# Performance work log

Hardware: AMD Instinct MI355X
Metric: run time of the kernel (lower is better)

Reference implementation:

```python
import jax, jax.numpy as jnp
import numpy as np

D_MODEL = 768
NUM_HEADS = 48
HEAD_CH = D_MODEL // NUM_HEADS  # 16
INNER = 3 * D_MODEL
BATCH = 2
SEQLEN = 2048
SKIP = 1.0
EPS = 1e-6


def setup_inputs() -> dict:
    key = jax.random.key(0)
    ks = jax.random.split(key, 9)
    s_in = 1.0 / np.sqrt(D_MODEL)
    s_out = 1.0 / np.sqrt(D_MODEL)
    return {
        "inputs": jax.random.normal(ks[0], (BATCH, SEQLEN, D_MODEL), jnp.float32),
        "w_in": jax.random.normal(ks[1], (INNER, D_MODEL), jnp.float32) * s_in,
        "b_in": jax.random.normal(ks[2], (INNER,), jnp.float32) * 0.01,
        "w_sf": jax.random.normal(ks[3], (INNER, 3), jnp.float32) * 0.3,  # depthwise conv kernel
        "b_sf": jax.random.normal(ks[4], (INNER,), jnp.float32) * 0.01,
        "h": jax.random.normal(ks[5], (NUM_HEADS, SEQLEN), jnp.float32) * 0.02,  # long filter
        "norm_w": jnp.ones((D_MODEL,), jnp.float32),
        "w_out": jax.random.normal(ks[6], (D_MODEL, D_MODEL), jnp.float32) * s_out,
        "b_out": jax.random.normal(ks[7], (D_MODEL,), jnp.float32) * 0.01,
    }


def reference(inputs, w_in, b_in, w_sf, b_sf, h, norm_w, w_out, b_out):
    B, L, D = inputs.shape
    N, HC = NUM_HEADS, HEAD_CH
    # in_proj: [B, L, 3D]
    u = jnp.einsum('bld,ed->ble', inputs, w_in) + b_in
    u = jnp.transpose(u, (0, 2, 1))  # [B, 3D, L]
    # causal depthwise conv1d, kernel 3, left pad 2
    up = jnp.pad(u, ((0, 0), (0, 0), (2, 0)))
    uc = (w_sf[:, 0:1] * up[:, :, 0:L]
          + w_sf[:, 1:2] * up[:, :, 1:L + 1]
          + w_sf[:, 2:3] * up[:, :, 2:L + 2]
          + b_sf[:, None])  # [B, 3D, L]
    uc = uc.reshape(B, N, 3 * HC, L)
    x0 = uc[:, :, 0:HC, :]            # q  [B, N, HC, L]
    x1 = uc[:, :, HC:2 * HC, :]       # k  [B, N, HC, L]
    v = uc[:, :, 2 * HC:3 * HC, :]    # v  [B, N, HC, L]
    # outer product: [B, HC_i, HC_j, N, L]
    kv = jnp.einsum('bnil,bnjl->bijnl', x1, v)
    # FFT long convolution with h [N, L], broadcast over b,i,j
    fft_size = 2 * L
    k_f = jnp.fft.rfft(h, n=fft_size) / fft_size        # [N, L+1]
    u_f = jnp.fft.rfft(kv, n=fft_size, axis=-1)         # [B, HC, HC, N, L+1]
    hkv = jnp.fft.irfft(u_f * k_f, n=fft_size, axis=-1, norm='forward')[..., :L]
    # contract with q: [B, L, N, HC_j]
    qhkv = jnp.einsum('bijnl,bnil->blnj', hkv, x0)
    y = qhkv.reshape(B, L, D)
    # RMSNorm
    ms = jnp.mean(jnp.square(y), axis=-1, keepdims=True)
    y = y * jax.lax.rsqrt(ms + EPS) * norm_w
    # out_proj + skip
    y = jnp.einsum('bld,ed->ble', y, w_out) + b_out
    return y + inputs * SKIP
```

## Files before the change

kernel.cpp:

```cpp
#include <hip/hip_runtime.h>
#include <hip/hip_bf16.h>
#include <stdint.h>

typedef __bf16 bf16;
typedef __bf16 bf16x4 __attribute__((ext_vector_type(4)));
typedef __bf16 bf16x8 __attribute__((ext_vector_type(8)));
typedef float f32x4 __attribute__((ext_vector_type(4)));
typedef float f32x16 __attribute__((ext_vector_type(16)));

#define D_MODEL 768
#define NUM_HEADS 48
#define HEAD_CH 16
#define INNER 2304
#define BATCH 2
#define SEQLEN 2048
#define M_ROWS (BATCH * SEQLEN)
#define EPSF 1e-6f

__device__ inline void gload_lds16(const void* g, void* l) {
  __builtin_amdgcn_global_load_lds((__attribute__((address_space(1))) void*)(g),
                                   (__attribute__((address_space(3))) void*)(l),
                                   16, 0, 0);
}

__global__ __launch_bounds__(256) void cvt2_f32_bf16(
    const float* __restrict__ a, bf16* __restrict__ da, int na4,
    const float* __restrict__ b, bf16* __restrict__ db, int nb4) {
  int j = blockIdx.x * 256 + threadIdx.x;
  const float* s;
  bf16* d;
  if (j < na4) {
    s = a; d = da;
  } else {
    j -= na4;
    if (j >= nb4) return;
    s = b; d = db;
  }
  const float4 v = ((const float4*)s)[j];
  bf16x4 o;
  o[0] = (bf16)v.x; o[1] = (bf16)v.y; o[2] = (bf16)v.z; o[3] = (bf16)v.w;
  ((bf16x4*)d)[j] = o;
}

__global__ __launch_bounds__(256) void cvt_f32_bf16(
    const float* __restrict__ src, bf16* __restrict__ dst, int n4) {
  const int i = blockIdx.x * 256 + threadIdx.x;
  if (i < n4) {
    const float4 v = ((const float4*)src)[i];
    bf16x4 o;
    o[0] = (bf16)v.x; o[1] = (bf16)v.y; o[2] = (bf16)v.z; o[3] = (bf16)v.w;
    ((bf16x4*)dst)[i] = o;
  }
}

template <int TM, int TN, int NCOLS, bool ADD_SKIP, typename CT>
__global__ __launch_bounds__(256) void gemm_bt(
    const bf16* __restrict__ A, const bf16* __restrict__ W,
    const float* __restrict__ bias, const float* __restrict__ skip,
    CT* __restrict__ C, int K) {
  constexpr int MI = TM / 32;
  constexpr int NI = TN / 32;
  __shared__ __align__(16) bf16 As[TM * 32];
  __shared__ __align__(16) bf16 Bs[TN * 32];
  const int t = threadIdx.x;
  const int lane = t & 63, w = t >> 6;
  const int wm = (w >> 1) * (TM / 2), wn = (w & 1) * (TN / 2);
  const int row16 = lane & 15, quad = lane >> 4;
  const int m0 = blockIdx.x * TM, n0 = blockIdx.y * TN;

  f32x4 zero4 = {0.f, 0.f, 0.f, 0.f};
  f32x4 acc[MI][NI];
#pragma unroll
  for (int mi = 0; mi < MI; ++mi)
#pragma unroll
    for (int ni = 0; ni < NI; ++ni) acc[mi][ni] = zero4;

  const int arow = t >> 2;
  const int acol = (t & 3) * 8;
  const bf16* Ab = A + (size_t)m0 * K;
  const bf16* Wb = W + (size_t)n0 * K;

  for (int kt = 0; kt < K; kt += 32) {
    gload_lds16(Ab + (size_t)arow * K + kt + acol, As + t * 8);
    if (TM == 128)
      gload_lds16(Ab + (size_t)(64 + arow) * K + kt + acol, As + 2048 + t * 8);
    gload_lds16(Wb + (size_t)arow * K + kt + acol, Bs + t * 8);
    if (TN == 128)
      gload_lds16(Wb + (size_t)(64 + arow) * K + kt + acol, Bs + 2048 + t * 8);
    __syncthreads();

    bf16x8 af[MI], wf[NI];
#pragma unroll
    for (int mi = 0; mi < MI; ++mi)
      af[mi] = *(const bf16x8*)&As[(wm + mi * 16 + row16) * 32 + quad * 8];
#pragma unroll
    for (int ni = 0; ni < NI; ++ni)
      wf[ni] = *(const bf16x8*)&Bs[(wn + ni * 16 + row16) * 32 + quad * 8];
#pragma unroll
    for (int mi = 0; mi < MI; ++mi)
#pragma unroll
      for (int ni = 0; ni < NI; ++ni)
        acc[mi][ni] = __builtin_amdgcn_mfma_f32_16x16x32_bf16(
            af[mi], wf[ni], acc[mi][ni], 0, 0, 0);
    __syncthreads();
  }

#pragma unroll
  for (int mi = 0; mi < MI; ++mi) {
#pragma unroll
    for (int ni = 0; ni < NI; ++ni) {
      const int col = n0 + wn + ni * 16 + row16;
      const float bv = bias[col];
#pragma unroll
      for (int r = 0; r < 4; ++r) {
        const int row = m0 + wm + mi * 16 + quad * 4 + r;
        float v = acc[mi][ni][r] + bv;
        if (ADD_SKIP) v += skip[(size_t)row * NCOLS + col];
        C[(size_t)row * NCOLS + col] = (CT)v;
      }
    }
  }
}

__global__ __launch_bounds__(256) void conv_qkv(
    const bf16* __restrict__ u, const float* __restrict__ w_sf,
    const float* __restrict__ b_sf, bf16* __restrict__ qq,
    bf16* __restrict__ kk, bf16* __restrict__ vv) {
  const int nh = blockIdx.x, b = blockIdx.y, lc = blockIdx.z;
  const int l0 = lc * 128;
  __shared__ __align__(8) bf16 ut[130 * 48];
  const int t = threadIdx.x;
  for (int i = t; i < 130 * 12; i += 256) {
    const int lr = i / 12, qd = i % 12;
    const int l = l0 - 2 + lr;
    uint2 val;
    val.x = 0u; val.y = 0u;
    if (l >= 0)
      val = *(const uint2*)&u[(size_t)(b * SEQLEN + l) * INNER + nh * 48 + qd * 4];
    *(uint2*)&ut[lr * 48 + qd * 4] = val;
  }
  __syncthreads();
  const size_t bn = (size_t)(b * NUM_HEADS + nh);
#pragma unroll
  for (int s = 0; s < 2; ++s) {
    bf16* dst = (s == 0) ? qq : kk;
    const int cb = s * 16;
    for (int i = t; i < 128 * 16; i += 256) {
      const int c = i & 15, lr = i >> 4;
      const int e = nh * 48 + cb + c;
      const float val = w_sf[e * 3 + 0] * (float)ut[lr * 48 + cb + c] +
                        w_sf[e * 3 + 1] * (float)ut[(lr + 1) * 48 + cb + c] +
                        w_sf[e * 3 + 2] * (float)ut[(lr + 2) * 48 + cb + c] +
                        b_sf[e];
      dst[(bn * SEQLEN + l0 + lr) * 16 + c] = (bf16)val;
    }
  }
  for (int i = t; i < 128 * 16; i += 256) {
    const int lr = i & 127, c = i >> 7;
    const int e = nh * 48 + 32 + c;
    const float val = w_sf[e * 3 + 0] * (float)ut[lr * 48 + 32 + c] +
                      w_sf[e * 3 + 1] * (float)ut[(lr + 1) * 48 + 32 + c] +
                      w_sf[e * 3 + 2] * (float)ut[(lr + 2) * 48 + 32 + c] +
                      b_sf[e];
    vv[(bn * 16 + c) * SEQLEN + l0 + lr] = (bf16)val;
  }
}

__global__ __launch_bounds__(256) void attn_kernel(
    const bf16* __restrict__ qq, const bf16* __restrict__ kk,
    const bf16* __restrict__ vv, const float* __restrict__ hg,
    float* __restrict__ y) {
  const int nh = blockIdx.x, b = blockIdx.y;
  const int q32 = (int)gridDim.z - 1 - (int)blockIdx.z;
  const int l0 = q32 * 32;
  __shared__ __align__(16) float hs[32 + SEQLEN];
  __shared__ __align__(16) bf16 st[4 * 32 * 40];
  const int t = threadIdx.x;
  const int n4 = (l0 + 64) >> 2;
  for (int i = t; i < n4; i += 256) {
    float4 val = {0.f, 0.f, 0.f, 0.f};
    if (i >= 8) val = ((const float4*)(hg + nh * SEQLEN))[i - 8];
    ((float4*)hs)[i] = val;
  }
  __syncthreads();

  const int w = t >> 6, lane = t & 63;
  const int l31 = lane & 31, hi = lane >> 5;
  const int row16 = lane & 15, quad = lane >> 4;
  const size_t bn = (size_t)(b * NUM_HEADS + nh);
  const bf16* qb = qq + bn * SEQLEN * 16;
  const bf16* kb = kk + bn * SEQLEN * 16;
  const bf16* vb = vv + bn * 16 * SEQLEN;

  bf16x8 zf;
#pragma unroll
  for (int j = 0; j < 8; ++j) zf[j] = (bf16)0.f;
  const f32x4 zacc4 = {0.f, 0.f, 0.f, 0.f};
  f32x16 zacc16;
#pragma unroll
  for (int j = 0; j < 16; ++j) zacc16[j] = 0.f;

  const bf16x8 qf = *(const bf16x8*)&qb[(l0 + l31) * 16 + hi * 8];

  f32x4 o0 = zacc4, o1 = zacc4;
  bf16* sw = &st[w * 32 * 40];

  int mc = w * 32;
  bf16x8 kf = zf, vf = zf;
  if (mc <= l0) {
    kf = *(const bf16x8*)&kb[(mc + l31) * 16 + hi * 8];
    vf = *(const bf16x8*)&vb[row16 * SEQLEN + mc + quad * 8];
  }
  for (; mc <= l0; mc += 128) {
    const int mn = mc + 128;
    bf16x8 kf2 = zf, vf2 = zf;
    if (mn <= l0) {
      kf2 = *(const bf16x8*)&kb[(mn + l31) * 16 + hi * 8];
      vf2 = *(const bf16x8*)&vb[row16 * SEQLEN + mn + quad * 8];
    }
    f32x16 s = __builtin_amdgcn_mfma_f32_32x32x16_bf16(kf, qf, zacc16, 0, 0, 0);

    const int d0 = 32 + (l0 - mc) + l31 - 4 * hi;
#pragma unroll
    for (int g = 0; g < 4; ++g) {
      const float* hp = &hs[d0 - 8 * g - 3];
      bf16x4 pk;
      pk[0] = (bf16)(s[4 * g + 0] * hp[3]);
      pk[1] = (bf16)(s[4 * g + 1] * hp[2]);
      pk[2] = (bf16)(s[4 * g + 2] * hp[1]);
      pk[3] = (bf16)(s[4 * g + 3] * hp[0]);
      *(bf16x4*)&sw[l31 * 40 + 8 * g + 4 * hi] = pk;
    }
    asm volatile("s_waitcnt lgkmcnt(0)" ::: "memory");
    const bf16x8 sf0 = *(const bf16x8*)&sw[row16 * 40 + quad * 8];
    const bf16x8 sf1 = *(const bf16x8*)&sw[(row16 + 16) * 40 + quad * 8];
    o0 = __builtin_amdgcn_mfma_f32_16x16x32_bf16(sf0, vf, o0, 0, 0, 0);
    o1 = __builtin_amdgcn_mfma_f32_16x16x32_bf16(sf1, vf, o1, 0, 0, 0);
    asm volatile("" ::: "memory");
    kf = kf2; vf = vf2;
  }

  float* ob = (float*)&st[w * 32 * 40];
#pragma unroll
  for (int r = 0; r < 4; ++r) {
    ob[(quad * 4 + r) * 16 + row16] = o0[r];
    ob[(quad * 4 + r + 16) * 16 + row16] = o1[r];
  }
  __syncthreads();
  for (int i = t; i < 32 * 16; i += 256) {
    const int l = i >> 4, j = i & 15;
    float sum = 0.f;
#pragma unroll
    for (int ww = 0; ww < 4; ++ww)
      sum += ((const float*)&st[ww * 32 * 40])[l * 16 + j];
    y[((size_t)(b * SEQLEN + l0 + l) * NUM_HEADS + nh) * 16 + j] = sum;
  }
}

__global__ __launch_bounds__(256) void rmsnorm_k(
    const float* __restrict__ y, const float* __restrict__ nw,
    bf16* __restrict__ yn) {
  const int row = blockIdx.x;
  const int t = threadIdx.x;
  const float* yr = y + (size_t)row * D_MODEL;
  const float v0 = yr[t];
  const float v1 = yr[t + 256];
  const float v2 = yr[t + 512];
  float ss = v0 * v0 + v1 * v1 + v2 * v2;
#pragma unroll
  for (int off = 32; off >= 1; off >>= 1) ss += __shfl_down(ss, off, 64);
  __shared__ float red[4];
  if ((t & 63) == 0) red[t >> 6] = ss;
  __syncthreads();
  const float tot = red[0] + red[1] + red[2] + red[3];
  const float r = rsqrtf(tot * (1.f / 768.f) + EPSF);
  bf16* yo = yn + (size_t)row * D_MODEL;
  yo[t] = (bf16)(v0 * r * nw[t]);
  yo[t + 256] = (bf16)(v1 * r * nw[t + 256]);
  yo[t + 512] = (bf16)(v2 * r * nw[t + 512]);
}

extern "C" void kernel_launch(void* const* d_in, const int* in_sizes, int n_in,
                              void* d_out, int out_size, void* d_ws,
                              size_t ws_size, hipStream_t stream) {
  const float* inputs = (const float*)d_in[0];
  const float* w_in = (const float*)d_in[1];
  const float* b_in = (const float*)d_in[2];
  const float* w_sf = (const float*)d_in[3];
  const float* b_sf = (const float*)d_in[4];
  const float* hb = (const float*)d_in[5];
  const float* norm_w = (const float*)d_in[6];
  const float* w_out = (const float*)d_in[7];
  const float* b_out = (const float*)d_in[8];

  char* ws = (char*)d_ws;
  const size_t U_B = (size_t)M_ROWS * INNER * 2;
  const size_t V_B = (size_t)BATCH * NUM_HEADS * HEAD_CH * SEQLEN * 2;
  const size_t SLOT_B = (size_t)M_ROWS * D_MODEL * 2;
  bf16* u = (bf16*)(ws);
  bf16* wout16 = (bf16*)(ws);
  bf16* yn = (bf16*)(ws + (2 << 20));
  bf16* v = (bf16*)(ws + U_B);
  bf16* in16 = (bf16*)(ws + U_B + V_B);
  bf16* k16 = in16;
  bf16* win16 = (bf16*)(ws + U_B + V_B + SLOT_B);
  bf16* q16 = win16;
  float* y = (float*)d_out;
  float* out = (float*)d_out;

  const int n4_in = M_ROWS * D_MODEL / 4;
  const int n4_win = INNER * D_MODEL / 4;
  const int n4_wout = D_MODEL * D_MODEL / 4;
  hipLaunchKernelGGL(cvt2_f32_bf16, dim3((n4_in + n4_win + 255) / 256),
                     dim3(256), 0, stream, inputs, in16, n4_in, w_in, win16,
                     n4_win);

  hipLaunchKernelGGL((gemm_bt<128, 128, INNER, false, bf16>), dim3(32, 18),
                     dim3(256), 0, stream, in16, win16, b_in,
                     (const float*)nullptr, u, 768);
  hipLaunchKernelGGL(conv_qkv, dim3(48, 2, 16), dim3(256), 0, stream, u, w_sf,
                     b_sf, q16, k16, v);
  hipLaunchKernelGGL(cvt_f32_bf16, dim3((n4_wout + 255) / 256), dim3(256), 0,
                     stream, w_out, wout16, n4_wout);
  hipLaunchKernelGGL(attn_kernel, dim3(48, 2, 64), dim3(256), 0, stream, q16,
                     k16, v, hb, y);
  hipLaunchKernelGGL(rmsnorm_k, dim3(M_ROWS), dim3(256), 0, stream, y, norm_w,
                     yn);
  hipLaunchKernelGGL((gemm_bt<64, 64, D_MODEL, true, float>), dim3(64, 12),
                     dim3(256), 0, stream, yn, wout16, b_out, inputs, out,
                     768);
}
```

Before: 190.4 us.

## Pair causal query tiles per block and store attention output in bf16

Each attention block now handles two query tiles, z and 63-z, with two waves per tile. This balances the causal workload across blocks and halves the grid. The intermediate y buffer is written as bf16 to a workspace slot instead of fp32, which cuts the write and read traffic between the attention and RMSNorm kernels. The cost is some reduced precision before normalization, plus a workspace offset that must not overlap live buffers.

```diff
diff --git a/kernel.cpp b/kernel.cpp
--- a/kernel.cpp
+++ b/kernel.cpp
@@ -169,14 +169,14 @@
 __global__ __launch_bounds__(256) void attn_kernel(
     const bf16* __restrict__ qq, const bf16* __restrict__ kk,
     const bf16* __restrict__ vv, const float* __restrict__ hg,
-    float* __restrict__ y) {
+    bf16* __restrict__ y) {
   const int nh = blockIdx.x, b = blockIdx.y;
-  const int q32 = (int)gridDim.z - 1 - (int)blockIdx.z;
-  const int l0 = q32 * 32;
+  const int z = blockIdx.z;
+  const int qa = z, qb = 63 - z;
   __shared__ __align__(16) float hs[32 + SEQLEN];
   __shared__ __align__(16) bf16 st[4 * 32 * 40];
   const int t = threadIdx.x;
-  const int n4 = (l0 + 64) >> 2;
+  const int n4 = (qb * 32 + 64) >> 2;
   for (int i = t; i < n4; i += 256) {
     float4 val = {0.f, 0.f, 0.f, 0.f};
     if (i >= 8) val = ((const float4*)(hg + nh * SEQLEN))[i - 8];
@@ -185,10 +185,12 @@
   __syncthreads();
 
   const int w = t >> 6, lane = t & 63;
+  const int tile = w >> 1, p = w & 1;
+  const int l0 = (tile ? qb : qa) * 32;
   const int l31 = lane & 31, hi = lane >> 5;
   const int row16 = lane & 15, quad = lane >> 4;
   const size_t bn = (size_t)(b * NUM_HEADS + nh);
-  const bf16* qb = qq + bn * SEQLEN * 16;
+  const bf16* qb_ = qq + bn * SEQLEN * 16;
   const bf16* kb = kk + bn * SEQLEN * 16;
   const bf16* vb = vv + bn * 16 * SEQLEN;
 
@@ -200,19 +202,19 @@
 #pragma unroll
   for (int j = 0; j < 16; ++j) zacc16[j] = 0.f;
 
-  const bf16x8 qf = *(const bf16x8*)&qb[(l0 + l31) * 16 + hi * 8];
+  const bf16x8 qf = *(const bf16x8*)&qb_[(l0 + l31) * 16 + hi * 8];
 
   f32x4 o0 = zacc4, o1 = zacc4;
   bf16* sw = &st[w * 32 * 40];
 
-  int mc = w * 32;
+  int mc = p * 32;
   bf16x8 kf = zf, vf = zf;
   if (mc <= l0) {
     kf = *(const bf16x8*)&kb[(mc + l31) * 16 + hi * 8];
     vf = *(const bf16x8*)&vb[row16 * SEQLEN + mc + quad * 8];
   }
-  for (; mc <= l0; mc += 128) {
-    const int mn = mc + 128;
+  for (; mc <= l0; mc += 64) {
+    const int mn = mc + 64;
     bf16x8 kf2 = zf, vf2 = zf;
     if (mn <= l0) {
       kf2 = *(const bf16x8*)&kb[(mn + l31) * 16 + hi * 8];
@@ -247,25 +249,28 @@
     ob[(quad * 4 + r + 16) * 16 + row16] = o1[r];
   }
   __syncthreads();
+  const float* oa0 = (const float*)&st[0 * 32 * 40];
+  const float* oa1 = (const float*)&st[1 * 32 * 40];
+  const float* ob0 = (const float*)&st[2 * 32 * 40];
+  const float* ob1 = (const float*)&st[3 * 32 * 40];
   for (int i = t; i < 32 * 16; i += 256) {
     const int l = i >> 4, j = i & 15;
-    float sum = 0.f;
-#pragma unroll
-    for (int ww = 0; ww < 4; ++ww)
-      sum += ((const float*)&st[ww * 32 * 40])[l * 16 + j];
-    y[((size_t)(b * SEQLEN + l0 + l) * NUM_HEADS + nh) * 16 + j] = sum;
+    const float sa = oa0[i] + oa1[i];
+    const float sb = ob0[i] + ob1[i];
+    y[((size_t)(b * SEQLEN + qa * 32 + l) * NUM_HEADS + nh) * 16 + j] = (bf16)sa;
+    y[((size_t)(b * SEQLEN + qb * 32 + l) * NUM_HEADS + nh) * 16 + j] = (bf16)sb;
   }
 }
 
 __global__ __launch_bounds__(256) void rmsnorm_k(
-    const float* __restrict__ y, const float* __restrict__ nw,
+    const bf16* __restrict__ y, const float* __restrict__ nw,
     bf16* __restrict__ yn) {
   const int row = blockIdx.x;
   const int t = threadIdx.x;
-  const float* yr = y + (size_t)row * D_MODEL;
-  const float v0 = yr[t];
-  const float v1 = yr[t + 256];
-  const float v2 = yr[t + 512];
+  const bf16* yr = y + (size_t)row * D_MODEL;
+  const float v0 = (float)yr[t];
+  const float v1 = (float)yr[t + 256];
+  const float v2 = (float)yr[t + 512];
   float ss = v0 * v0 + v1 * v1 + v2 * v2;
 #pragma unroll
   for (int off = 32; off >= 1; off >>= 1) ss += __shfl_down(ss, off, 64);
@@ -300,12 +305,12 @@
   bf16* u = (bf16*)(ws);
   bf16* wout16 = (bf16*)(ws);
   bf16* yn = (bf16*)(ws + (2 << 20));
+  bf16* y16 = (bf16*)(ws + (9 << 20));
   bf16* v = (bf16*)(ws + U_B);
   bf16* in16 = (bf16*)(ws + U_B + V_B);
   bf16* k16 = in16;
   bf16* win16 = (bf16*)(ws + U_B + V_B + SLOT_B);
   bf16* q16 = win16;
-  float* y = (float*)d_out;
   float* out = (float*)d_out;
 
   const int n4_in = M_ROWS * D_MODEL / 4;
@@ -322,10 +327,10 @@
                      b_sf, q16, k16, v);
   hipLaunchKernelGGL(cvt_f32_bf16, dim3((n4_wout + 255) / 256), dim3(256), 0,
                      stream, w_out, wout16, n4_wout);
-  hipLaunchKernelGGL(attn_kernel, dim3(48, 2, 64), dim3(256), 0, stream, q16,
-                     k16, v, hb, y);
-  hipLaunchKernelGGL(rmsnorm_k, dim3(M_ROWS), dim3(256), 0, stream, y, norm_w,
-                     yn);
+  hipLaunchKernelGGL(attn_kernel, dim3(48, 2, 32), dim3(256), 0, stream, q16,
+                     k16, v, hb, y16);
+  hipLaunchKernelGGL(rmsnorm_k, dim3(M_ROWS), dim3(256), 0, stream, y16,
+                     norm_w, yn);
   hipLaunchKernelGGL((gemm_bt<64, 64, D_MODEL, true, float>), dim3(64, 12),
                      dim3(256), 0, stream, yn, wout16, b_out, inputs, out,
                      768);
```

Result: no change. 193.1 us (+1.4%).
